# Performance work log

Measured on AMD Instinct MI355X. Metric: run time of the kernel, lower is better.

## Reference

```python
import jax, jax.numpy as jnp
import numpy as np
import math

B, N, H, D = 2, 2048, 16, 64
NUM_BUCKETS, MAX_DIST = 32, 128
MODEL = H * D


def _rel_pos_bucket(rel, num_buckets, max_distance):
    # T5-style bucketing (bidirectional): half the buckets for sign, half log-spaced.
    nb = num_buckets // 2
    ret = (rel >= 0).astype(jnp.int32) * nb
    n = jnp.abs(rel)
    max_exact = nb // 2
    is_small = n < max_exact
    n_safe = jnp.maximum(n, 1).astype(jnp.float32)
    val_large = max_exact + (
        jnp.log(n_safe / max_exact) / math.log(max_distance / max_exact) * (nb - max_exact)
    ).astype(jnp.int32)
    val_large = jnp.minimum(val_large, nb - 1)
    return ret + jnp.where(is_small, n, val_large)


def _rel_pos_bias(rel_emb, n, m):
    q_pos = jnp.arange(m - n, m)
    k_pos = jnp.arange(m)
    rel = k_pos[None, :] - q_pos[:, None]            # [n, m]
    buckets = _rel_pos_bucket(rel, NUM_BUCKETS, MAX_DIST)
    bias = rel_emb[buckets]                          # [n, m, h]
    return bias.transpose(2, 0, 1)[None]             # [1, h, n, m]


def setup_inputs() -> dict:
    key = jax.random.key(0)
    ks = jax.random.split(key, 6)
    return {
        "q": jax.random.normal(ks[0], (B, N, MODEL), dtype=jnp.float32),
        "k": jax.random.normal(ks[1], (B, N, MODEL), dtype=jnp.float32),
        "v": jax.random.normal(ks[2], (B, N, MODEL), dtype=jnp.float32),
        "rel_emb": jax.random.normal(ks[3], (NUM_BUCKETS, H), dtype=jnp.float32) * 0.05,
        "w_out": jax.random.normal(ks[4], (MODEL, MODEL), dtype=jnp.float32) * (MODEL ** -0.5),
        "b_out": jax.random.normal(ks[5], (MODEL,), dtype=jnp.float32) * 0.02,
    }


def reference(q, k, v, rel_emb, w_out, b_out):
    b, n, _ = q.shape
    split = lambda x: x.reshape(b, n, H, D).transpose(0, 2, 1, 3)  # b h n d
    qh, kh, vh = split(q), split(k), split(v)
    sim = jnp.einsum('bhnd,bhmd->bhnm', qh, kh)
    sim = (sim + _rel_pos_bias(rel_emb, n, n)) * (D ** -0.5)  # note: scale AFTER bias, as in source
    attn = jax.nn.softmax(sim, axis=-1)
    out = jnp.einsum('bhnm,bhmd->bhnd', attn, vh)
    out = out.transpose(0, 2, 1, 3).reshape(b, n, H * D)
    return out @ w_out.T + b_out
```

## Files before the change

kernel.cpp:

```cpp
#include <hip/hip_runtime.h>

#define BB 2
#define NN 2048
#define HH 16
#define MODEL 1024
#define CSC 0.18033688011112042f

typedef short bf16x8 __attribute__((ext_vector_type(8)));
typedef float f32x4 __attribute__((ext_vector_type(4)));
typedef int i32x2 __attribute__((ext_vector_type(2)));

__device__ __forceinline__ unsigned short f2bf(float x) {
  unsigned int u = __builtin_bit_cast(unsigned int, x);
  u += 0x7fffu + ((u >> 16) & 1u);
  return (unsigned short)(u >> 16);
}

__device__ __forceinline__ unsigned int pack_bf2(float a, float b) {
  unsigned int ua = __builtin_bit_cast(unsigned int, a) + 0x8000u;
  unsigned int ub = __builtin_bit_cast(unsigned int, b) + 0x8000u;
  return __builtin_amdgcn_perm(ub, ua, 0x07060302u);
}

__device__ __forceinline__ unsigned int pack2_rne(float a, float b) {
  return (unsigned int)f2bf(a) | ((unsigned int)f2bf(b) << 16);
}

__device__ __forceinline__ float fast_exp2(float x) {
#if __has_builtin(__builtin_amdgcn_exp2f)
  return __builtin_amdgcn_exp2f(x);
#else
  return exp2f(x);
#endif
}

__device__ __forceinline__ f32x4 mfma16(bf16x8 a, bf16x8 b, f32x4 c) {
  return __builtin_amdgcn_mfma_f32_16x16x32_bf16(a, b, c, 0, 0, 0);
}

__device__ __forceinline__ void async_copy16(void* lds_base, const void* g) {
  __builtin_amdgcn_global_load_lds(
      (const __attribute__((address_space(1))) void*)g,
      (__attribute__((address_space(3))) void*)lds_base, 16, 0, 0);
}

__global__ void prep_kernel(const float* __restrict__ k, const float* __restrict__ w,
                            const float* __restrict__ v, const float* __restrict__ rel_emb,
                            unsigned short* __restrict__ kb, unsigned short* __restrict__ wb,
                            unsigned short* __restrict__ vt, float* __restrict__ biasTab) {
  __shared__ unsigned short tile[64][65];
  const int NK4 = BB * NN * MODEL / 4;
  const int blk = blockIdx.x;
  if (blk < 5120) {
    int i = blk * 256 + threadIdx.x;
    const float* src;
    unsigned short* dst;
    int j = i;
    if (i < NK4) {
      src = k; dst = kb;
    } else {
      src = w; dst = wb; j = i - NK4;
    }
    float4 f = reinterpret_cast<const float4*>(src)[j];
    ushort4 u;
    u.x = f2bf(f.x); u.y = f2bf(f.y); u.z = f2bf(f.z); u.w = f2bf(f.w);
    reinterpret_cast<ushort4*>(dst)[j] = u;
  } else if (blk < 6144) {
    const int blk2 = blk - 5120;
    const int n0 = (blk2 & 31) * 64;
    const int bh = blk2 >> 5;
    const int b = bh >> 4, h = bh & 15;
    const int c = threadIdx.x & 63;
    const int r = threadIdx.x >> 6;
#pragma unroll
    for (int i = 0; i < 16; ++i) {
      int nl = r * 16 + i;
      tile[c][nl] = f2bf(v[((long)(b * NN + n0 + nl)) * MODEL + h * 64 + c]);
    }
    __syncthreads();
#pragma unroll
    for (int i = 0; i < 16; ++i) {
      int d = r * 16 + i;
      vt[((long)(bh * 64 + d)) * NN + n0 + c] = tile[d][c];
    }
  } else {
    int idx = (blk - 6144) * 256 + threadIdx.x;
    if (idx >= 4095) return;
    int rel = idx - 2047;
    int nn = rel < 0 ? -rel : rel;
    int bucket;
    if (nn < 8) {
      bucket = nn;
    } else {
      float val = logf((float)nn * 0.125f) / logf(16.0f) * 8.0f;
      int vl = 8 + (int)val;
      if (vl > 15) vl = 15;
      bucket = vl;
    }
    if (rel >= 0) bucket += 16;
#pragma unroll
    for (int h = 0; h < 16; ++h)
      biasTab[h * 4095 + idx] = rel_emb[bucket * 16 + h] * CSC - 12.0f;
  }
}

__global__ __launch_bounds__(256, 2) void flash14(
    const float* __restrict__ qf32, const unsigned short* __restrict__ kb,
    const unsigned short* __restrict__ vtb, const float* __restrict__ biasTab,
    unsigned short* __restrict__ attn) {
  __shared__ __align__(16) float obuf[4 * 64 * 68];
  __shared__ __align__(16) float scratch[512];

  const int i = blockIdx.x;
  const int bh = (i & 7) * 4 + ((i >> 3) >> 5);
  const int qt = (i >> 3) & 31;
  const int b = bh >> 4, h = bh & 15;
  const int q0 = qt * 64;
  const int tid = threadIdx.x, w = tid >> 6, lane = tid & 63;
  const int g = lane >> 4, c = lane & 15;

  const float* btab = biasTab + h * 4095 + 2047;
  for (int j = tid; j < 441; j += 256) scratch[j] = btab[j - 220];
  const float cPos = btab[200], cNeg = btab[-200];
  __syncthreads();

  bf16x8 qf0[4], qf1[4];
  const float* qbase = qf32 + ((long)(b * NN + q0)) * MODEL + h * 64;
#pragma unroll
  for (int nt = 0; nt < 4; ++nt) {
    const float* r = qbase + (16 * nt + c) * MODEL + 8 * g;
    float4 f0 = *reinterpret_cast<const float4*>(r);
    float4 f1 = *reinterpret_cast<const float4*>(r + 4);
    float4 f2 = *reinterpret_cast<const float4*>(r + 32);
    float4 f3 = *reinterpret_cast<const float4*>(r + 36);
    qf0[nt] = __builtin_bit_cast(bf16x8, uint4{pack2_rne(f0.x, f0.y), pack2_rne(f0.z, f0.w),
                                               pack2_rne(f1.x, f1.y), pack2_rne(f1.z, f1.w)});
    qf1[nt] = __builtin_bit_cast(bf16x8, uint4{pack2_rne(f2.x, f2.y), pack2_rne(f2.z, f2.w),
                                               pack2_rne(f3.x, f3.y), pack2_rne(f3.z, f3.w)});
  }

  const unsigned short* kbase = kb + ((long)b * NN) * MODEL + h * 64;
  const unsigned short* vbase = vtb + ((long)bh * 64) * NN;

  f32x4 o[4][4];
  float l_p[4] = {0.f, 0.f, 0.f, 0.f};
#pragma unroll
  for (int mt = 0; mt < 4; ++mt)
#pragma unroll
    for (int nt = 0; nt < 4; ++nt) o[mt][nt] = f32x4{0.f, 0.f, 0.f, 0.f};

  for (int it = 0; it < 8; ++it) {
    const int kt = w + 4 * it;
    bf16x8 kf0[4], kf1[4];
    const unsigned short* krow = kbase + (long)(kt * 64) * MODEL;
#pragma unroll
    for (int mt = 0; mt < 4; ++mt) {
      const unsigned short* r = krow + (16 * mt + c) * MODEL + 8 * g;
      kf0[mt] = *reinterpret_cast<const bf16x8*>(r);
      kf1[mt] = *reinterpret_cast<const bf16x8*>(r + 32);
    }
    bf16x8 vf0[4], vf1[4];
    const unsigned short* vrow = vbase + kt * 64;
#pragma unroll
    for (int mt = 0; mt < 4; ++mt) {
      const unsigned short* r = vrow + (long)(16 * mt + c) * NN + 8 * g;
      vf0[mt] = *reinterpret_cast<const bf16x8*>(r);
      vf1[mt] = *reinterpret_cast<const bf16x8*>(r + 32);
    }
    const int lo = kt * 64 - q0 - 63, hi = kt * 64 + 63 - q0;
    const bool sat = (lo >= 91 || hi <= -91);
    const float cb = (lo >= 91) ? cPos : cNeg;

    bf16x8 pb0, pb1;
#pragma unroll
    for (int nt = 0; nt < 4; ++nt) {
      f32x4 s[4];
#pragma unroll
      for (int mt = 0; mt < 4; ++mt) {
        s[mt] = mfma16(kf0[mt], qf0[nt], f32x4{0.f, 0.f, 0.f, 0.f});
        s[mt] = mfma16(kf1[mt], qf1[nt], s[mt]);
      }
      if (nt > 0) {
#pragma unroll
        for (int mt = 0; mt < 4; ++mt) {
          o[mt][nt - 1] = mfma16(vf0[mt], pb0, o[mt][nt - 1]);
          o[mt][nt - 1] = mfma16(vf1[mt], pb1, o[mt][nt - 1]);
        }
      }
      if (sat) {
#pragma unroll
        for (int mt = 0; mt < 4; ++mt)
#pragma unroll
          for (int rr = 0; rr < 4; ++rr) s[mt][rr] = s[mt][rr] * CSC + cb;
      } else {
        const int base = kt * 64 + 4 * g - q0 - 16 * nt - c + 220;
#pragma unroll
        for (int mt = 0; mt < 4; ++mt)
#pragma unroll
          for (int rr = 0; rr < 4; ++rr)
            s[mt][rr] = s[mt][rr] * CSC + scratch[base + 16 * mt + rr];
      }
      float sum = 0.f;
      unsigned int pk[4][2];
#pragma unroll
      for (int mt = 0; mt < 4; ++mt) {
        const float p0 = fast_exp2(s[mt][0]);
        const float p1 = fast_exp2(s[mt][1]);
        const float p2 = fast_exp2(s[mt][2]);
        const float p3 = fast_exp2(s[mt][3]);
        sum += (p0 + p1) + (p2 + p3);
        pk[mt][0] = pack_bf2(p0, p1);
        pk[mt][1] = pack_bf2(p2, p3);
      }
      l_p[nt] += sum;
      unsigned int d0, d1, d2, d3, d4, d5, d6, d7;
      {
        i32x2 x, y;
        x = __builtin_amdgcn_permlane32_swap((int)pk[0][0], (int)pk[1][0], false, false);
        y = __builtin_amdgcn_permlane16_swap(x[0], x[1], false, false);
        d0 = (unsigned int)y[0]; d2 = (unsigned int)y[1];
        x = __builtin_amdgcn_permlane32_swap((int)pk[0][1], (int)pk[1][1], false, false);
        y = __builtin_amdgcn_permlane16_swap(x[0], x[1], false, false);
        d1 = (unsigned int)y[0]; d3 = (unsigned int)y[1];
        x = __builtin_amdgcn_permlane32_swap((int)pk[2][0], (int)pk[3][0], false, false);
        y = __builtin_amdgcn_permlane16_swap(x[0], x[1], false, false);
        d4 = (unsigned int)y[0]; d6 = (unsigned int)y[1];
        x = __builtin_amdgcn_permlane32_swap((int)pk[2][1], (int)pk[3][1], false, false);
        y = __builtin_amdgcn_permlane16_swap(x[0], x[1], false, false);
        d5 = (unsigned int)y[0]; d7 = (unsigned int)y[1];
      }
      pb0 = __builtin_bit_cast(bf16x8, uint4{d0, d1, d2, d3});
      pb1 = __builtin_bit_cast(bf16x8, uint4{d4, d5, d6, d7});
    }
#pragma unroll
    for (int mt = 0; mt < 4; ++mt) {
      o[mt][3] = mfma16(vf0[mt], pb0, o[mt][3]);
      o[mt][3] = mfma16(vf1[mt], pb1, o[mt][3]);
    }
  }

  __syncthreads();
  float* ob = obuf + w * 64 * 68;
#pragma unroll
  for (int nt = 0; nt < 4; ++nt) {
    ob[(16 * nt + c) * 68 + 64 + g] = l_p[nt];
#pragma unroll
    for (int mt = 0; mt < 4; ++mt)
      *reinterpret_cast<f32x4*>(&ob[(16 * nt + c) * 68 + 16 * mt + 4 * g]) = o[mt][nt];
  }
  __syncthreads();

  const int qr = 16 * w + c;
  float l = 0.f;
#pragma unroll
  for (int u = 0; u < 4; ++u)
#pragma unroll
    for (int gg = 0; gg < 4; ++gg) l += obuf[(u * 64 + qr) * 68 + 64 + gg];
  const float inv = 1.f / l;

  float acc[16];
#pragma unroll
  for (int j = 0; j < 16; ++j) acc[j] = 0.f;
#pragma unroll
  for (int u = 0; u < 4; ++u) {
    const float* src = obuf + (u * 64 + qr) * 68;
    f32x4 r0 = *reinterpret_cast<const f32x4*>(&src[8 * g]);
    f32x4 r1 = *reinterpret_cast<const f32x4*>(&src[8 * g + 4]);
    f32x4 r2 = *reinterpret_cast<const f32x4*>(&src[32 + 8 * g]);
    f32x4 r3 = *reinterpret_cast<const f32x4*>(&src[32 + 8 * g + 4]);
#pragma unroll
    for (int j = 0; j < 4; ++j) {
      acc[j] += r0[j];
      acc[4 + j] += r1[j];
      acc[8 + j] += r2[j];
      acc[12 + j] += r3[j];
    }
  }
  unsigned int od[8];
#pragma unroll
  for (int t = 0; t < 8; ++t) od[t] = pack_bf2(acc[2 * t] * inv, acc[2 * t + 1] * inv);
  unsigned short* orow = attn + ((long)(b * NN + q0 + qr)) * MODEL + h * 64;
  *reinterpret_cast<uint4*>(orow + 8 * g) = uint4{od[0], od[1], od[2], od[3]};
  *reinterpret_cast<uint4*>(orow + 32 + 8 * g) = uint4{od[4], od[5], od[6], od[7]};
}

__global__ void proj_gemm_kernel(const unsigned short* __restrict__ A,
                                 const unsigned short* __restrict__ Bw,
                                 const float* __restrict__ bias,
                                 float* __restrict__ out) {
  __shared__ __align__(16) unsigned short At[2][128 * 64];
  __shared__ __align__(16) unsigned short Bt[2][64 * 64];
  int bm0 = blockIdx.x * 128, bn0 = blockIdx.y * 64;
  int tid = threadIdx.x, w = tid >> 6, lane = tid & 63;
  int g = lane >> 4, c = lane & 15;
  int m0 = (w & 1) * 64, n0 = (w >> 1) * 32;

  f32x4 acc[4][2];
#pragma unroll
  for (int mi = 0; mi < 4; ++mi)
#pragma unroll
    for (int nj = 0; nj < 2; ++nj) acc[mi][nj] = f32x4{0.f, 0.f, 0.f, 0.f};

  int rloc = lane >> 3, p = lane & 7;

  auto stage = [&](int buf, int kt) {
#pragma unroll
    for (int t = 0; t < 4; ++t) {
      int row = w * 32 + t * 8 + rloc;
      async_copy16(&At[buf][(w * 32 + t * 8) * 64],
                   A + (long)(bm0 + row) * 1024 + kt * 64 + (p ^ rloc) * 8);
    }
#pragma unroll
    for (int t = 0; t < 2; ++t) {
      int row = w * 16 + t * 8 + rloc;
      async_copy16(&Bt[buf][(w * 16 + t * 8) * 64],
                   Bw + (long)(bn0 + row) * 1024 + kt * 64 + (p ^ rloc) * 8);
    }
  };

  int cur = 0;
  stage(0, 0);
  for (int kt = 0; kt < 16; ++kt) {
    __syncthreads();
    if (kt < 15) stage(cur ^ 1, kt + 1);

    bf16x8 af0[4], af1[4], bf0[2], bf1[2];
#pragma unroll
    for (int mi = 0; mi < 4; ++mi) {
      int row = m0 + 16 * mi + c, sw = row & 7;
      af0[mi] = *reinterpret_cast<const bf16x8*>(&At[cur][row * 64 + (g ^ sw) * 8]);
      af1[mi] = *reinterpret_cast<const bf16x8*>(&At[cur][row * 64 + ((4 + g) ^ sw) * 8]);
    }
#pragma unroll
    for (int nj = 0; nj < 2; ++nj) {
      int row = n0 + 16 * nj + c, sw = row & 7;
      bf0[nj] = *reinterpret_cast<const bf16x8*>(&Bt[cur][row * 64 + (g ^ sw) * 8]);
      bf1[nj] = *reinterpret_cast<const bf16x8*>(&Bt[cur][row * 64 + ((4 + g) ^ sw) * 8]);
    }
#pragma unroll
    for (int mi = 0; mi < 4; ++mi)
#pragma unroll
      for (int nj = 0; nj < 2; ++nj) {
        acc[mi][nj] = mfma16(af0[mi], bf0[nj], acc[mi][nj]);
        acc[mi][nj] = mfma16(af1[mi], bf1[nj], acc[mi][nj]);
      }
    cur ^= 1;
  }

#pragma unroll
  for (int mi = 0; mi < 4; ++mi)
#pragma unroll
    for (int nj = 0; nj < 2; ++nj)
#pragma unroll
      for (int r = 0; r < 4; ++r) {
        int row = bm0 + m0 + mi * 16 + 4 * g + r;
        int col = bn0 + n0 + nj * 16 + c;
        out[(long)row * 1024 + col] = acc[mi][nj][r] + bias[col];
      }
}

extern "C" void kernel_launch(void* const* d_in, const int* in_sizes, int n_in,
                              void* d_out, int out_size, void* d_ws, size_t ws_size,
                              hipStream_t stream) {
  const float* q = (const float*)d_in[0];
  const float* k = (const float*)d_in[1];
  const float* v = (const float*)d_in[2];
  const float* rel_emb = (const float*)d_in[3];
  const float* w_out = (const float*)d_in[4];
  const float* b_out = (const float*)d_in[5];
  float* out = (float*)d_out;

  char* ws = (char*)d_ws;
  unsigned short* kb   = (unsigned short*)(ws + (8u << 20));
  unsigned short* vt   = (unsigned short*)(ws + (16u << 20));
  unsigned short* attn = (unsigned short*)(ws + (24u << 20));
  unsigned short* wb   = (unsigned short*)(ws + (32u << 20));
  float* biasTab       = (float*)(ws + (34u << 20));

  hipLaunchKernelGGL(prep_kernel, dim3(6161), dim3(256), 0, stream,
                     k, w_out, v, rel_emb, kb, wb, vt, biasTab);
  hipLaunchKernelGGL(flash14, dim3(1024), dim3(256), 0, stream,
                     q, kb, vt, biasTab, attn);
  hipLaunchKernelGGL(proj_gemm_kernel, dim3(32, 16), dim3(256), 0, stream,
                     attn, wb, b_out, out);
}
```

Measured before the change: 188.5 us.

## Double-buffer K tiles in LDS via async copies with swizzled layout

K tiles are now staged per wave into a double-buffered, XOR-swizzled LDS region (reusing obuf) with async global-to-LDS copies. The copy for the next tile is issued before the current one is computed, with explicit vmcnt waits, so global-load latency overlaps with MFMA work. The loop is fully unrolled. This adds LDS traffic and relies on hand-tuned waitcnt counts, and it is only safe if obuf is not in use during the loop.

```diff
diff --git a/kernel.cpp b/kernel.cpp
--- a/kernel.cpp
+++ b/kernel.cpp
@@ -104,7 +104,7 @@
   }
 }
 
-__global__ __launch_bounds__(256, 2) void flash14(
+__global__ __launch_bounds__(256, 2) void flash15(
     const float* __restrict__ qf32, const unsigned short* __restrict__ kb,
     const unsigned short* __restrict__ vtb, const float* __restrict__ biasTab,
     unsigned short* __restrict__ attn) {
@@ -142,6 +142,10 @@
   const unsigned short* kbase = kb + ((long)b * NN) * MODEL + h * 64;
   const unsigned short* vbase = vtb + ((long)bh * 64) * NN;
 
+  unsigned short* kst = reinterpret_cast<unsigned short*>(obuf) + w * 8192;
+  const int ksub = lane >> 3;
+  const int kcol = ((lane & 7) ^ ksub) * 8;
+
   f32x4 o[4][4];
   float l_p[4] = {0.f, 0.f, 0.f, 0.f};
 #pragma unroll
@@ -149,16 +153,22 @@
 #pragma unroll
     for (int nt = 0; nt < 4; ++nt) o[mt][nt] = f32x4{0.f, 0.f, 0.f, 0.f};
 
+  auto stageK = [&](int kt, int buf) {
+    unsigned short* dst = kst + buf * 4096;
+    const unsigned short* src = kbase + (long)(kt * 64) * MODEL;
+#pragma unroll
+    for (int t = 0; t < 8; ++t)
+      async_copy16(dst + t * 512, src + (long)(8 * t + ksub) * MODEL + kcol);
+  };
+
+  stageK(w, 0);
+
+#pragma unroll
   for (int it = 0; it < 8; ++it) {
     const int kt = w + 4 * it;
-    bf16x8 kf0[4], kf1[4];
-    const unsigned short* krow = kbase + (long)(kt * 64) * MODEL;
-#pragma unroll
-    for (int mt = 0; mt < 4; ++mt) {
-      const unsigned short* r = krow + (16 * mt + c) * MODEL + 8 * g;
-      kf0[mt] = *reinterpret_cast<const bf16x8*>(r);
-      kf1[mt] = *reinterpret_cast<const bf16x8*>(r + 32);
-    }
+    const int buf = it & 1;
+    if (it < 7) stageK(kt + 4, buf ^ 1);
+
     bf16x8 vf0[4], vf1[4];
     const unsigned short* vrow = vbase + kt * 64;
 #pragma unroll
@@ -167,6 +177,26 @@
       vf0[mt] = *reinterpret_cast<const bf16x8*>(r);
       vf1[mt] = *reinterpret_cast<const bf16x8*>(r + 32);
     }
+
+    __builtin_amdgcn_sched_barrier(0);
+    if (it < 7) {
+      asm volatile("s_waitcnt vmcnt(16)" ::: "memory");
+    } else {
+      asm volatile("s_waitcnt vmcnt(8)" ::: "memory");
+    }
+    __builtin_amdgcn_sched_barrier(0);
+
+    bf16x8 kf0[4], kf1[4];
+    {
+      const unsigned short* base = kst + buf * 4096;
+#pragma unroll
+      for (int mt = 0; mt < 4; ++mt) {
+        const int r = 16 * mt + c, sw = c & 7;
+        kf0[mt] = *reinterpret_cast<const bf16x8*>(base + r * 64 + ((g ^ sw) * 8));
+        kf1[mt] = *reinterpret_cast<const bf16x8*>(base + r * 64 + (((4 + g) ^ sw) * 8));
+      }
+    }
+
     const int lo = kt * 64 - q0 - 63, hi = kt * 64 + 63 - q0;
     const bool sat = (lo >= 91 || hi <= -91);
     const float cb = (lo >= 91) ? cPos : cNeg;
@@ -379,7 +409,7 @@
 
   hipLaunchKernelGGL(prep_kernel, dim3(6161), dim3(256), 0, stream,
                      k, w_out, v, rel_emb, kb, wb, vt, biasTab);
-  hipLaunchKernelGGL(flash14, dim3(1024), dim3(256), 0, stream,
+  hipLaunchKernelGGL(flash15, dim3(1024), dim3(256), 0, stream,
                      q, kb, vt, biasTab, attn);
   hipLaunchKernelGGL(proj_gemm_kernel, dim3(32, 16), dim3(256), 0, stream,
                      attn, wb, b_out, out);
```

After: 411.7 us. 118% more time.
